# Performance work log

Measured on AMD Instinct MI355X. Metric: run time of the kernel, lower is better.

## Reference

```python
import jax, jax.numpy as jnp
import numpy as np

N_USER = 150_000
M_ITEM = 30_000
N_NODES = N_USER + M_ITEM
D = 64                      # embedding_dim
N_LAYERS = 3                # gcn_layer_number
E = 600_000                 # user-item interactions (symmetric nnz = 2E)
B = 1024
NUM_RATE, NUM_GENRE, NUM_DIR, NUM_ACT = 6, 25, 2186, 8030
NUM_GENDER, NUM_AGE, NUM_OCC, NUM_ZIP = 2, 7, 21, 3402
H1, H2 = 64, 64             # first/second fc hidden dims
FC1_IN = D * 10


def setup_inputs() -> dict:
    key = jax.random.key(0)
    ks = jax.random.split(key, 24)
    # aux features: 0/1 values are valid indices for every categorical field
    aux_info = jax.random.randint(ks[0], (B, 10246), 0, 2, dtype=jnp.int32)
    user_ids = jax.random.randint(ks[1], (B,), 0, N_USER, dtype=jnp.int32)
    item_ids = jax.random.randint(ks[2], (B,), 0, M_ITEM, dtype=jnp.int32)
    # bipartite graph: random interactions, symmetric normalized adjacency
    u = jax.random.randint(ks[3], (E,), 0, N_USER, dtype=jnp.int32)
    i = jax.random.randint(ks[4], (E,), 0, M_ITEM, dtype=jnp.int32) + N_USER
    graph_row = jnp.concatenate([u, i])
    graph_col = jnpph = jnp.concatenate([i, u]) if False else jnp.concatenate([i, u])
    deg = jax.ops.segment_sum(jnp.ones((2 * E,), jnp.float32), graph_row, num_segments=N_NODES)
    dinv = jnp.where(deg > 0, jax.lax.rsqrt(jnp.maximum(deg, 1.0)), 0.0)
    graph_val = dinv[graph_row] * dinv[graph_col]
    s = 0.1
    nrm = lambda k, shp: (jax.random.normal(k, shp, jnp.float32) * s)
    return {
        "aux_info": aux_info, "user_ids": user_ids, "item_ids": item_ids,
        "graph_row": graph_row, "graph_col": graph_col, "graph_val": graph_val,
        "rate_tab": nrm(ks[5], (NUM_RATE, D)),
        "genre_W": nrm(ks[6], (NUM_GENRE, D)),
        "director_W": nrm(ks[7], (NUM_DIR, D)),
        "actor_W": nrm(ks[8], (NUM_ACT, D)),
        "gender_tab": nrm(ks[9], (NUM_GENDER, D)),
        "age_tab": nrm(ks[10], (NUM_AGE, D)),
        "occ_tab": nrm(ks[11], (NUM_OCC, D)),
        "area_tab": nrm(ks[12], (NUM_ZIP, D)),
        "user_rel": nrm(ks[13], (N_USER, D)),
        "item_rel": nrm(ks[14], (M_ITEM, D)),
        "fc1_W": nrm(ks[15], (FC1_IN, H1)), "fc1_b": jnp.zeros((H1,), jnp.float32),
        "fc2_W": nrm(ks[16], (H1, H2)), "fc2_b": jnp.zeros((H2,), jnp.float32),
        "out_W": nrm(ks[17], (H2, 1)), "out_b": jnp.zeros((1,), jnp.float32),
    }


def _lightgcn(user_rel, item_rel, row, col, val):
    # LightGCN: repeated SpMM D^-1/2 A D^-1/2 @ emb, mean over layer outputs
    emb = jnp.concatenate([user_rel, item_rel], axis=0)      # [N, D]
    acc = emb
    for _ in range(N_LAYERS):
        emb = jax.ops.segment_sum(val[:, None] * emb[col], row, num_segments=N_NODES)
        acc = acc + emb
    light = acc / (N_LAYERS + 1)
    return light[:N_USER], light[N_USER:]


def _multi_hot(idx_int, W):
    x = idx_int.astype(jnp.float32)
    return (x @ W) / jnp.sum(x, axis=1, keepdims=True)


def reference(aux_info, user_ids, item_ids, graph_row, graph_col, graph_val,
              rate_tab, genre_W, director_W, actor_W,
              gender_tab, age_tab, occ_tab, area_tab,
              user_rel, item_rel,
              fc1_W, fc1_b, fc2_W, fc2_b, out_W, out_b):
    rate_idx = aux_info[:, 0]
    genre_idx = aux_info[:, 1:26]
    director_idx = aux_info[:, 26:2212]
    actor_idx = aux_info[:, 2212:10242]
    gender_idx = aux_info[:, 10242]
    age_idx = aux_info[:, 10243]
    occ_idx = aux_info[:, 10244]
    area_idx = aux_info[:, 10245]

    item_emb = jnp.concatenate([
        rate_tab[rate_idx],
        _multi_hot(genre_idx, genre_W),
        _multi_hot(director_idx, director_W),
        _multi_hot(actor_idx, actor_W),
    ], axis=1)                                               # [B, 4D]
    user_emb = jnp.concatenate([
        gender_tab[gender_idx], age_tab[age_idx],
        occ_tab[occ_idx], area_tab[area_idx],
    ], axis=1)                                               # [B, 4D]

    all_users, all_items = _lightgcn(user_rel, item_rel, graph_row, graph_col, graph_val)
    X = jnp.concatenate([item_emb, user_emb,
                         all_users[user_ids], all_items[item_ids]], axis=1)  # [B, 10D]
    X = jax.nn.relu(X @ fc1_W + fc1_b)
    X = jax.nn.relu(X @ fc2_W + fc2_b)
    return X @ out_W + out_b                                 # [B, 1]
```

## Files before the change

kernel.cpp:

```cpp
#include <hip/hip_runtime.h>
#include <hip/hip_bf16.h>
#include <hip/hip_fp16.h>

#define N_USER 150000
#define M_ITEM 30000
#define N_NODES 180000
#define E2 1200000
#define BATCH 1024
#define AUX_W 10246
#define KP_G 32
#define KP_D 2208
#define KP_A 8064
#define NBKT 265

typedef __attribute__((ext_vector_type(8))) short short8;
typedef __attribute__((ext_vector_type(4))) float f32x4;

__device__ __forceinline__ int bucket_of(int r) {
    return r < N_USER ? (r >> 10) : 147 + ((r - N_USER) >> 8);
}

__device__ __forceinline__ int detect_f32(const void* probe) {
    float v = __bfloat162float(((const __hip_bfloat16*)probe)[threadIdx.x & 63]);
    unsigned long long m = __ballot(!(fabsf(v) < 1000.0f));
    return __popcll(m) > 8;
}

struct CvtSeg { const void* src; float* dst; int n; int blk0; };
struct CvtBatch { CvtSeg seg[16]; };

__global__ void __launch_bounds__(256) k_cvt_batch(CvtBatch cb, const void* probe) {
    int isf32 = detect_f32(probe);
    int blk = blockIdx.x;
    int si = 0;
    #pragma unroll
    for (int i = 0; i < 16; ++i) if (blk >= cb.seg[i].blk0) si = i;
    const CvtSeg sg = cb.seg[si];
    int i = (blk - sg.blk0) * 256 + threadIdx.x;
    if (i >= sg.n) return;
    if (isf32) sg.dst[i] = ((const float*)sg.src)[i];
    else       sg.dst[i] = __bfloat162float(((const __hip_bfloat16*)sg.src)[i]);
}

__global__ void __launch_bounds__(256) k_cvt_emb(const void* rawU, const void* rawI,
                                                 const float* __restrict__ dinv,
                                                 __half* __restrict__ emb,
                                                 float* __restrict__ tacc,
                                                 const int* __restrict__ uids,
                                                 const int* __restrict__ iids, int cvtN) {
    int isf32 = detect_f32(rawU);
    if ((int)blockIdx.x >= cvtN) {
        int lane = threadIdx.x & 63;
        int t = (blockIdx.x - cvtN) * 4 + (threadIdx.x >> 6);
        const void* src; size_t ri;
        if (t < BATCH) { src = rawU; ri = (size_t)uids[t]; }
        else           { src = rawI; ri = (size_t)iids[t - BATCH]; }
        float v;
        if (isf32) v = ((const float*)src)[ri * 64 + lane];
        else       v = __bfloat162float(((const __hip_bfloat16*)src)[ri * 64 + lane]);
        tacc[(size_t)t * 64 + lane] = v;
        return;
    }
    int q = blockIdx.x * 256 + threadIdx.x;
    if (q >= N_NODES * 16) return;
    int r = q >> 4;
    const void* src; size_t qq;
    if (r < N_USER) { src = rawU; qq = (size_t)q; }
    else            { src = rawI; qq = (size_t)q - (size_t)N_USER * 16; }
    float d = dinv[r];
    float4 v;
    if (isf32) {
        v = ((const float4*)src)[qq];
    } else {
        ushort4 u = ((const ushort4*)src)[qq];
        v.x = __bfloat162float(*(__hip_bfloat16*)&u.x);
        v.y = __bfloat162float(*(__hip_bfloat16*)&u.y);
        v.z = __bfloat162float(*(__hip_bfloat16*)&u.z);
        v.w = __bfloat162float(*(__hip_bfloat16*)&u.w);
    }
    __half h0 = __float2half(v.x * d), h1 = __float2half(v.y * d);
    __half h2 = __float2half(v.z * d), h3 = __float2half(v.w * d);
    ushort4 o = { *(unsigned short*)&h0, *(unsigned short*)&h1,
                  *(unsigned short*)&h2, *(unsigned short*)&h3 };
    ((ushort4*)emb)[(size_t)q] = o;
}

__global__ void __launch_bounds__(256) k_wt(const void* Wg, const void* Wd, const void* Wa,
                                            unsigned short* WtG, unsigned short* WtD, unsigned short* WtA,
                                            const void* probe) {
    int isf32 = detect_f32(probe);
    int t = blockIdx.x * 256 + threadIdx.x;
    if (t >= (KP_G + KP_D + KP_A) * 64) return;
    int kp = t >> 6, n = t & 63;
    int k, K; const void* src; unsigned short* dst;
    if (kp < KP_G)              { k = kp;                K = 25;   src = Wg; dst = WtG; }
    else if (kp < KP_G + KP_D)  { k = kp - KP_G;         K = 2186; src = Wd; dst = WtD; }
    else                        { k = kp - KP_G - KP_D;  K = 8030; src = Wa; dst = WtA; }
    unsigned short v = 0;
    if (k < K) {
        if (isf32) {
            __hip_bfloat16 h = __float2bfloat16(((const float*)src)[(size_t)k * 64 + n]);
            v = *(unsigned short*)&h;
        } else {
            v = ((const unsigned short*)src)[(size_t)k * 64 + n];
        }
    }
    dst[(((size_t)(k >> 5) * 64 + n) * 4 + ((k >> 3) & 3)) * 8 + (k & 7)] = v;
}

__global__ void __launch_bounds__(256) k_zero(int* p, int n) {
    int i = blockIdx.x * 256 + threadIdx.x;
    if (i < n) p[i] = 0;
}

__global__ void __launch_bounds__(256) k_bcnt(const int* __restrict__ grow, int* __restrict__ bucket_tot) {
    __shared__ int h[NBKT];
    int tid = threadIdx.x;
    for (int i = tid; i < NBKT; i += 256) h[i] = 0;
    __syncthreads();
    int idx0 = blockIdx.x * 4096;
    #pragma unroll
    for (int k = 0; k < 16; ++k) {
        int i = idx0 + k * 256 + tid;
        if (i < E2) atomicAdd(&h[bucket_of(grow[i])], 1);
    }
    __syncthreads();
    for (int i = tid; i < NBKT; i += 256) if (h[i]) atomicAdd(&bucket_tot[i], h[i]);
}

__global__ void __launch_bounds__(512) k_bscan(const int* __restrict__ bucket_tot,
                                               int* __restrict__ bucket_base,
                                               int* __restrict__ bucketcur,
                                               int* __restrict__ offs) {
    __shared__ int s[512];
    int tid = threadIdx.x;
    s[tid] = (tid < NBKT) ? bucket_tot[tid] : 0;
    __syncthreads();
    for (int off = 1; off < 512; off <<= 1) {
        int v = (tid >= off) ? s[tid - off] : 0;
        __syncthreads();
        s[tid] += v;
        __syncthreads();
    }
    int excl = tid ? s[tid - 1] : 0;
    bucket_base[tid] = excl;
    if (tid < NBKT) bucketcur[tid] = excl;
    if (tid == 0) offs[N_NODES] = E2;
}

__global__ void __launch_bounds__(256) k_p1(const int* __restrict__ grow, const int* __restrict__ gcol,
                                            int* __restrict__ bucketcur, int2* __restrict__ binned) {
    __shared__ int h1[NBKT], base1[NBKT];
    int tid = threadIdx.x;
    for (int i = tid; i < NBKT; i += 256) h1[i] = 0;
    __syncthreads();
    int idx0 = blockIdx.x * 4096;
    int r[16], c[16];
    #pragma unroll
    for (int k = 0; k < 16; ++k) {
        int i = idx0 + k * 256 + tid;
        if (i < E2) {
            r[k] = grow[i]; c[k] = gcol[i];
            atomicAdd(&h1[bucket_of(r[k])], 1);
        } else r[k] = -1;
    }
    __syncthreads();
    for (int i = tid; i < NBKT; i += 256) {
        base1[i] = h1[i] ? atomicAdd(&bucketcur[i], h1[i]) : 0;
        h1[i] = 0;
    }
    __syncthreads();
    #pragma unroll
    for (int k = 0; k < 16; ++k) {
        if (r[k] >= 0) {
            int b = bucket_of(r[k]);
            int p = base1[b] + atomicAdd(&h1[b], 1);
            binned[p] = make_int2(r[k], c[k]);
        }
    }
}

__global__ void __launch_bounds__(256) k_p2(const int2* __restrict__ binned, const int* __restrict__ bb,
                                            int* __restrict__ cols, int* __restrict__ offs,
                                            float* __restrict__ dinv, float* __restrict__ dsq,
                                            float* __restrict__ gsc) {
    __shared__ int h[1024];
    __shared__ int ws2[256];
    int b = blockIdx.x, tid = threadIdx.x;
    int r0, r1;
    if (b < 147) { r0 = b << 10; r1 = min((b + 1) << 10, N_USER); }
    else         { r0 = N_USER + ((b - 147) << 8); r1 = min(N_USER + ((b - 146) << 8), N_NODES); }
    int s0 = bb[b], e0 = bb[b + 1];
    for (int i = tid; i < 1024; i += 256) h[i] = 0;
    __syncthreads();
    for (int j = s0 + tid; j < e0; j += 256) atomicAdd(&h[binned[j].x - r0], 1);
    __syncthreads();
    int t0 = tid * 4;
    int a0 = h[t0], a1 = h[t0 + 1], a2 = h[t0 + 2], a3 = h[t0 + 3];
    ws2[tid] = a0 + a1 + a2 + a3;
    __syncthreads();
    for (int off = 1; off < 256; off <<= 1) {
        int v = (tid >= off) ? ws2[tid - off] : 0;
        __syncthreads();
        ws2[tid] += v;
        __syncthreads();
    }
    int excl = tid ? ws2[tid - 1] : 0;
    int ex[4] = { excl, excl + a0, excl + a0 + a1, excl + a0 + a1 + a2 };
    int ac[4] = { a0, a1, a2, a3 };
    #pragma unroll
    for (int i = 0; i < 4; ++i) {
        int row = r0 + t0 + i;
        if (row < r1) {
            offs[row] = s0 + ex[i];
            float deg = (float)ac[i];
            bool nz = deg > 0.f;
            dinv[row] = nz ? rsqrtf(deg) : 0.f;
            dsq[row]  = nz ? 1.f / deg  : 0.f;
            gsc[row]  = nz ? sqrtf(deg) : 0.f;
        }
        h[t0 + i] = ex[i];
    }
    __syncthreads();
    for (int j = s0 + tid; j < e0; j += 256) {
        int2 e = binned[j];
        int p = s0 + atomicAdd(&h[e.x - r0], 1);
        cols[p] = e.y << 7;
    }
}

__global__ void __launch_bounds__(256) k_mark(const int* __restrict__ offs, const int* __restrict__ cols,
                                              const int* __restrict__ uids, const int* __restrict__ iids,
                                              int* __restrict__ mark, int* __restrict__ mark2) {
    int lane = threadIdx.x & 63;
    int t = blockIdx.x * 4 + (threadIdx.x >> 6);
    if (t >= 2048) return;
    int r = (t < BATCH) ? uids[t] : (N_USER + iids[t - BATCH]);
    if (lane == 0) { mark[r] = 1; mark2[r] = 1; }
    int s = offs[r], e = offs[r + 1];
    for (int j = s + lane; j < e; j += 64) mark[(unsigned)cols[j] >> 7] = 1;
}

__global__ void __launch_bounds__(256) k_mark2(const int* __restrict__ offs, const int* __restrict__ cols,
                                               const int* __restrict__ mark, int* __restrict__ mark2) {
    int lane = threadIdx.x & 63;
    int wid = blockIdx.x * 4 + (threadIdx.x >> 6);
    if (wid >= N_NODES) return;
    if (mark[wid] == 0) return;
    int s = offs[wid], e = offs[wid + 1];
    for (int j = s + lane; j < e; j += 64) mark2[(unsigned)cols[j] >> 7] = 1;
}

__global__ void __launch_bounds__(256, 8) k_spmv(const __half* __restrict__ src, __half* __restrict__ dst,
                                                 const int* __restrict__ offs, const int* __restrict__ cols,
                                                 const float* __restrict__ dsq, const int* __restrict__ mark,
                                                 int spmvN, float* __restrict__ tacc,
                                                 const int* __restrict__ uids, const int* __restrict__ iids,
                                                 const float* __restrict__ gsc) {
    int tid = threadIdx.x, lane = tid & 63;
    int blk = blockIdx.x;
    if (blk >= spmvN) {
        int t = (blk - spmvN) * 4 + (tid >> 6);
        int r = (t < BATCH) ? uids[t] : (N_USER + iids[t - BATCH]);
        tacc[(size_t)t * 64 + lane] += __half2float(src[(size_t)r * 64 + lane]) * gsc[r];
        return;
    }
    int wid = blk * 4 + (tid >> 6);
    if (wid >= N_NODES) return;
    if (mark && mark[wid] == 0) return;
    int s = offs[wid], e = offs[wid + 1];
    int p = lane & 31, ep = lane >> 5;
    const char* sb = (const char*)src + (p << 2);
    float ax = 0.f, ay = 0.f;
    int j0 = s;
    for (; j0 + 16 <= e; j0 += 16) {
        int c[8];
        #pragma unroll
        for (int u = 0; u < 8; ++u) c[u] = cols[j0 + 2 * u + ep];
        float2 v[8];
        #pragma unroll
        for (int u = 0; u < 8; ++u) v[u] = __half22float2(*(const __half2*)(sb + (size_t)(unsigned)c[u]));
        #pragma unroll
        for (int u = 0; u < 8; ++u) { ax += v[u].x; ay += v[u].y; }
    }
    if (j0 < e) {
        int c[8]; float w[8];
        #pragma unroll
        for (int u = 0; u < 8; ++u) {
            int j = j0 + 2 * u + ep;
            c[u] = cols[min(j, e - 1)];
            w[u] = (j < e) ? 1.f : 0.f;
        }
        float2 v[8];
        #pragma unroll
        for (int u = 0; u < 8; ++u) v[u] = __half22float2(*(const __half2*)(sb + (size_t)(unsigned)c[u]));
        #pragma unroll
        for (int u = 0; u < 8; ++u) { ax = fmaf(w[u], v[u].x, ax); ay = fmaf(w[u], v[u].y, ay); }
    }
    ax += __shfl_xor(ax, 32);
    ay += __shfl_xor(ay, 32);
    if (ep == 0) {
        float d = dsq[wid];
        *(__half2*)((char*)dst + ((size_t)wid << 7) + (p << 2)) = __floats2half2_rn(ax * d, ay * d);
    }
}

__global__ void __launch_bounds__(256) k_spmv3(const __half* __restrict__ src, float* __restrict__ tacc,
                                               const int* __restrict__ offs, const int* __restrict__ cols,
                                               const float* __restrict__ dinv, const float* __restrict__ gsc,
                                               const int* __restrict__ uids, const int* __restrict__ iids) {
    int tid = threadIdx.x, lane = tid & 63;
    int t = blockIdx.x * 4 + (tid >> 6);
    if (t >= 2048) return;
    int r = (t < BATCH) ? uids[t] : (N_USER + iids[t - BATCH]);
    int s = offs[r], e = offs[r + 1];
    int p = lane & 31, ep = lane >> 5;
    const char* sb = (const char*)src + (p << 2);
    float ax = 0.f, ay = 0.f;
    int j0 = s;
    for (; j0 + 16 <= e; j0 += 16) {
        int c[8];
        #pragma unroll
        for (int u = 0; u < 8; ++u) c[u] = cols[j0 + 2 * u + ep];
        float2 v[8];
        #pragma unroll
        for (int u = 0; u < 8; ++u) v[u] = __half22float2(*(const __half2*)(sb + (size_t)(unsigned)c[u]));
        #pragma unroll
        for (int u = 0; u < 8; ++u) { ax += v[u].x; ay += v[u].y; }
    }
    if (j0 < e) {
        int c[8]; float w[8];
        #pragma unroll
        for (int u = 0; u < 8; ++u) {
            int j = j0 + 2 * u + ep;
            c[u] = cols[min(j, e - 1)];
            w[u] = (j < e) ? 1.f : 0.f;
        }
        float2 v[8];
        #pragma unroll
        for (int u = 0; u < 8; ++u) v[u] = __half22float2(*(const __half2*)(sb + (size_t)(unsigned)c[u]));
        #pragma unroll
        for (int u = 0; u < 8; ++u) { ax = fmaf(w[u], v[u].x, ax); ay = fmaf(w[u], v[u].y, ay); }
    }
    ax += __shfl_xor(ax, 32);
    ay += __shfl_xor(ay, 32);
    if (ep == 0) {
        float2 self = __half22float2(*(const __half2*)((const char*)src + ((size_t)r << 7) + (p << 2)));
        float di = dinv[r], g = gsc[r];
        float* tp = tacc + (size_t)t * 64 + (p << 1);
        tp[0] += di * ax + g * self.x;
        tp[1] += di * ay + g * self.y;
    }
}

__global__ void __launch_bounds__(256) k_mhgemm(const int* __restrict__ aux,
                                                const unsigned short* __restrict__ WtG,
                                                const unsigned short* __restrict__ WtD,
                                                const unsigned short* __restrict__ WtA,
                                                float* __restrict__ Xmh, float* __restrict__ cntf) {
    int blk = blockIdx.x;
    int seg, rb, k0, klen, Kseg, auxoff;
    const unsigned short* Wt;
    if (blk < 16)      { seg = 0; rb = blk;                      k0 = 0;              klen = 25;                    Kseg = 25;   auxoff = 1;    Wt = WtG; }
    else if (blk < 96) { int t = blk - 16; seg = 1; rb = t & 15; k0 = (t >> 4) * 512; klen = min(512, 2186 - k0);   Kseg = 2186; auxoff = 26;   Wt = WtD; }
    else               { int t = blk - 96; seg = 2; rb = t & 15; k0 = (t >> 4) * 512; klen = min(512, 8030 - k0);   Kseg = 8030; auxoff = 2212; Wt = WtA; }
    int lane = threadIdx.x & 63, wave = threadIdx.x >> 6;
    int m = lane & 15, quad = lane >> 4;
    int row = rb * 64 + wave * 16 + m;
    const int* arow = aux + (size_t)row * AUX_W + auxoff;

    f32x4 acc0 = {0.f,0.f,0.f,0.f}, acc1 = acc0, acc2 = acc0, acc3 = acc0;
    float asum = 0.f;
    int nchunk = (klen + 31) >> 5;
    for (int kci = 0; kci < nchunk; ++kci) {
        int kb = k0 + kci * 32 + quad * 8;
        short8 af;
        if (kb + 8 <= Kseg) {
            #pragma unroll
            for (int j = 0; j < 8; ++j) {
                int x = arow[kb + j];
                af[j] = x ? (short)0x3F80 : (short)0;
                asum += (float)x;
            }
        } else {
            #pragma unroll
            for (int j = 0; j < 8; ++j) {
                int x = (kb + j < Kseg) ? arow[kb + j] : 0;
                af[j] = x ? (short)0x3F80 : (short)0;
                asum += (float)x;
            }
        }
        size_t kcg = (size_t)(k0 >> 5) + kci;
        const unsigned short* bp = Wt + ((kcg * 64 + m) * 4 + quad) * 8;
        short8 b0 = *(const short8*)(bp);
        short8 b1 = *(const short8*)(bp + 512);
        short8 b2 = *(const short8*)(bp + 1024);
        short8 b3 = *(const short8*)(bp + 1536);
        acc0 = __builtin_amdgcn_mfma_f32_16x16x32_bf16(af, b0, acc0, 0, 0, 0);
        acc1 = __builtin_amdgcn_mfma_f32_16x16x32_bf16(af, b1, acc1, 0, 0, 0);
        acc2 = __builtin_amdgcn_mfma_f32_16x16x32_bf16(af, b2, acc2, 0, 0, 0);
        acc3 = __builtin_amdgcn_mfma_f32_16x16x32_bf16(af, b3, acc3, 0, 0, 0);
    }
    asum += __shfl_xor(asum, 16);
    asum += __shfl_xor(asum, 32);
    if (quad == 0) atomicAdd(&cntf[seg * BATCH + row], asum);
    float* xbase = Xmh + ((size_t)seg * BATCH + rb * 64 + wave * 16 + quad * 4) * 64;
    #pragma unroll
    for (int reg = 0; reg < 4; ++reg) {
        float* xr = xbase + (size_t)reg * 64;
        atomicAdd(&xr[ 0 + m], acc0[reg]);
        atomicAdd(&xr[16 + m], acc1[reg]);
        atomicAdd(&xr[32 + m], acc2[reg]);
        atomicAdd(&xr[48 + m], acc3[reg]);
    }
}

__global__ void __launch_bounds__(256) k_mlp(const int* __restrict__ aux,
                                             const float* __restrict__ ratef, const float* __restrict__ genderf,
                                             const float* __restrict__ agef, const float* __restrict__ occf,
                                             const float* __restrict__ areaf, const float* __restrict__ tacc,
                                             const float* __restrict__ Xmh, const float* __restrict__ cntf,
                                             const float* __restrict__ W1, const float* __restrict__ b1,
                                             const float* __restrict__ W2, const float* __restrict__ b2,
                                             const float* __restrict__ Wo, const float* __restrict__ bo,
                                             void* __restrict__ out, const void* probe) {
    __shared__ float sx[4][640];
    __shared__ float sh[4][64];
    int isf32 = detect_f32(probe);
    int lane = threadIdx.x & 63, w = threadIdx.x >> 6;
    int b = blockIdx.x * 4 + w;
    const int* arow = aux + (size_t)b * AUX_W;
    float* xr = sx[w];
    xr[0   + lane] = ratef[arow[0] * 64 + lane];
    xr[64  + lane] = Xmh[((size_t)0 * BATCH + b) * 64 + lane] / cntf[0 * BATCH + b];
    xr[128 + lane] = Xmh[((size_t)1 * BATCH + b) * 64 + lane] / cntf[1 * BATCH + b];
    xr[192 + lane] = Xmh[((size_t)2 * BATCH + b) * 64 + lane] / cntf[2 * BATCH + b];
    xr[256 + lane] = genderf[arow[10242] * 64 + lane];
    xr[320 + lane] = agef[arow[10243] * 64 + lane];
    xr[384 + lane] = occf[arow[10244] * 64 + lane];
    xr[448 + lane] = areaf[arow[10245] * 64 + lane];
    xr[512 + lane] = tacc[(size_t)b * 64 + lane] * 0.25f;
    xr[576 + lane] = tacc[(size_t)(BATCH + b) * 64 + lane] * 0.25f;
    float acc = b1[lane];
    #pragma unroll 8
    for (int k = 0; k < 640; ++k) acc += xr[k] * W1[(size_t)k * 64 + lane];
    float h1 = fmaxf(acc, 0.f);
    sh[w][lane] = h1;
    float acc2 = b2[lane];
    #pragma unroll 8
    for (int j = 0; j < 64; ++j) acc2 += sh[w][j] * W2[(size_t)j * 64 + lane];
    float h2 = fmaxf(acc2, 0.f);
    float p = h2 * Wo[lane];
    #pragma unroll
    for (int off = 32; off; off >>= 1) p += __shfl_down(p, off);
    if (lane == 0) {
        float r = p + bo[0];
        if (isf32) ((float*)out)[b] = r;
        else       ((__hip_bfloat16*)out)[b] = __float2bfloat16(r);
    }
}

extern "C" void kernel_launch(void* const* d_in, const int* in_sizes, int n_in,
                              void* d_out, int out_size, void* d_ws, size_t ws_size,
                              hipStream_t stream) {
    const int* aux  = (const int*)d_in[0];
    const int* uids = (const int*)d_in[1];
    const int* iids = (const int*)d_in[2];
    const int* grow = (const int*)d_in[3];
    const int* gcol = (const int*)d_in[4];

    char* p = (char*)d_ws;
    auto alloc = [&](size_t bytes) -> char* {
        char* r = p;
        p += (bytes + 255) / 256 * 256;
        return r;
    };
    int*   mark        = (int*)alloc((size_t)180224 * 4);
    int*   mark2       = (int*)alloc((size_t)180224 * 4);
    int*   bucket_tot  = (int*)alloc(512 * 4);
    float* Xmh         = (float*)alloc((size_t)3 * BATCH * 64 * 4);
    float* cntf        = (float*)alloc((size_t)3 * BATCH * 4);
    const int ZERO_N   = 180224 + 180224 + 512 + 3 * BATCH * 64 + 3 * BATCH;
    int*   bucket_base = (int*)alloc(512 * 4);
    int*   bucketcur   = (int*)alloc(512 * 4);
    int*   offs        = (int*)alloc((size_t)180224 * 4);
    float* dinv        = (float*)alloc((size_t)180224 * 4);
    float* dsq         = (float*)alloc((size_t)180224 * 4);
    float* gsc         = (float*)alloc((size_t)180224 * 4);
    int2*  binned      = (int2*)alloc((size_t)E2 * 8);
    int*   cols        = (int*)alloc((size_t)E2 * 4);
    __half* embA       = (__half*)alloc((size_t)N_NODES * 64 * 2);
    __half* embB       = (__half*)alloc((size_t)N_NODES * 64 * 2);
    float* tacc        = (float*)alloc((size_t)2048 * 64 * 4);
    unsigned short* WtG = (unsigned short*)alloc((size_t)KP_G * 64 * 2);
    unsigned short* WtD = (unsigned short*)alloc((size_t)KP_D * 64 * 2);
    unsigned short* WtA = (unsigned short*)alloc((size_t)KP_A * 64 * 2);
    float* ratef   = (float*)alloc(384 * 4);
    float* genderf = (float*)alloc(128 * 4);
    float* agef    = (float*)alloc(448 * 4);
    float* occf    = (float*)alloc(1344 * 4);
    float* areaf   = (float*)alloc((size_t)217728 * 4);
    float* fc1W    = (float*)alloc((size_t)40960 * 4);
    float* fc1b    = (float*)alloc(64 * 4);
    float* fc2W    = (float*)alloc(4096 * 4);
    float* fc2b    = (float*)alloc(64 * 4);
    float* outW    = (float*)alloc(64 * 4);
    float* outb    = (float*)alloc(4);

    const void* probe = d_in[14];

    CvtBatch cb;
    int blk = 0, si = 0;
    auto addseg = [&](const void* s, float* d, int n) {
        cb.seg[si].src = s; cb.seg[si].dst = d; cb.seg[si].n = n; cb.seg[si].blk0 = blk;
        blk += (n + 255) / 256; ++si;
    };
    addseg(d_in[6],  ratef,   384);
    addseg(d_in[10], genderf, 128);
    addseg(d_in[11], agef,    448);
    addseg(d_in[12], occf,    1344);
    addseg(d_in[13], areaf,   217728);
    addseg(d_in[16], fc1W,   40960);
    addseg(d_in[17], fc1b,   64);
    addseg(d_in[18], fc2W,   4096);
    addseg(d_in[19], fc2b,   64);
    addseg(d_in[20], outW,   64);
    addseg(d_in[21], outb,   1);
    for (int i = si; i < 16; ++i) { cb.seg[i].src = nullptr; cb.seg[i].dst = nullptr; cb.seg[i].n = 0; cb.seg[i].blk0 = 0x7fffffff; }
    hipLaunchKernelGGL(k_cvt_batch, dim3(blk), dim3(256), 0, stream, cb, probe);

    hipLaunchKernelGGL(k_wt, dim3(((KP_G + KP_D + KP_A) * 64 + 255) / 256), dim3(256), 0, stream,
                       d_in[7], d_in[8], d_in[9], WtG, WtD, WtA, probe);

    hipLaunchKernelGGL(k_zero, dim3((ZERO_N + 255) / 256), dim3(256), 0, stream, mark, ZERO_N);

    hipLaunchKernelGGL(k_bcnt, dim3((E2 + 4095) / 4096), dim3(256), 0, stream, grow, bucket_tot);
    hipLaunchKernelGGL(k_bscan, dim3(1), dim3(512), 0, stream, bucket_tot, bucket_base, bucketcur, offs);
    hipLaunchKernelGGL(k_p1, dim3((E2 + 4095) / 4096), dim3(256), 0, stream, grow, gcol, bucketcur, binned);
    hipLaunchKernelGGL(k_p2, dim3(NBKT), dim3(256), 0, stream, binned, bucket_base, cols, offs, dinv, dsq, gsc);

    const int cvtN = (N_NODES * 16 + 255) / 256;
    hipLaunchKernelGGL(k_cvt_emb, dim3(cvtN + 512), dim3(256), 0, stream,
                       d_in[14], d_in[15], dinv, embA, tacc, uids, iids, cvtN);
    hipLaunchKernelGGL(k_mark, dim3(2048 / 4), dim3(256), 0, stream, offs, cols, uids, iids, mark, mark2);
    hipLaunchKernelGGL(k_mark2, dim3((N_NODES + 3) / 4), dim3(256), 0, stream, offs, cols, mark, mark2);

    const int spmvN = (N_NODES + 3) / 4;
    hipLaunchKernelGGL(k_spmv, dim3(spmvN), dim3(256), 0, stream,
                       embA, embB, offs, cols, dsq, mark2, spmvN, (float*)nullptr, uids, iids, gsc);
    hipLaunchKernelGGL(k_spmv, dim3(spmvN + 512), dim3(256), 0, stream,
                       embB, embA, offs, cols, dsq, mark, spmvN, tacc, uids, iids, gsc);
    hipLaunchKernelGGL(k_spmv3, dim3(2048 / 4), dim3(256), 0, stream,
                       embA, tacc, offs, cols, dinv, gsc, uids, iids);

    hipLaunchKernelGGL(k_mhgemm, dim3(352), dim3(256), 0, stream, aux, WtG, WtD, WtA, Xmh, cntf);
    hipLaunchKernelGGL(k_mlp, dim3(BATCH / 4), dim3(256), 0, stream,
                       aux, ratef, genderf, agef, occf, areaf, tacc, Xmh, cntf,
                       fc1W, fc1b, fc2W, fc2b, outW, outb, d_out, probe);
}
```

Measured before the change: 356.1 us.

## Fuse prep kernels and replace mark arrays with per-row start/end offsets

Merges the scalar-table conversion, weight transpose and bucket count into one prep kernel, and swaps the zero kernel for a memset. Row offsets are now stored as int2 start/end pairs, so the frontier masks for the pruned SpMV layers can be written as copied offsets in a second array, with empty ranges for skipped rows. The embedding conversion, frontier marking and the multi-hot GEMM now run in one fused launch. The aim is fewer launches and serialization points, at the cost of larger offset arrays and more complex block dispatch.

```diff
diff --git a/kernel.cpp b/kernel.cpp
--- a/kernel.cpp
+++ b/kernel.cpp
@@ -12,6 +12,8 @@
 #define KP_D 2208
 #define KP_A 8064
 #define NBKT 265
+#define WT_BLKS 2576
+#define BCNT_BLKS 293
 
 typedef __attribute__((ext_vector_type(8))) short short8;
 typedef __attribute__((ext_vector_type(4))) float f32x4;
@@ -29,96 +31,49 @@
 struct CvtSeg { const void* src; float* dst; int n; int blk0; };
 struct CvtBatch { CvtSeg seg[16]; };
 
-__global__ void __launch_bounds__(256) k_cvt_batch(CvtBatch cb, const void* probe) {
-    int isf32 = detect_f32(probe);
-    int blk = blockIdx.x;
-    int si = 0;
-    #pragma unroll
-    for (int i = 0; i < 16; ++i) if (blk >= cb.seg[i].blk0) si = i;
-    const CvtSeg sg = cb.seg[si];
-    int i = (blk - sg.blk0) * 256 + threadIdx.x;
-    if (i >= sg.n) return;
-    if (isf32) sg.dst[i] = ((const float*)sg.src)[i];
-    else       sg.dst[i] = __bfloat162float(((const __hip_bfloat16*)sg.src)[i]);
-}
-
-__global__ void __launch_bounds__(256) k_cvt_emb(const void* rawU, const void* rawI,
-                                                 const float* __restrict__ dinv,
-                                                 __half* __restrict__ emb,
-                                                 float* __restrict__ tacc,
-                                                 const int* __restrict__ uids,
-                                                 const int* __restrict__ iids, int cvtN) {
-    int isf32 = detect_f32(rawU);
-    if ((int)blockIdx.x >= cvtN) {
-        int lane = threadIdx.x & 63;
-        int t = (blockIdx.x - cvtN) * 4 + (threadIdx.x >> 6);
-        const void* src; size_t ri;
-        if (t < BATCH) { src = rawU; ri = (size_t)uids[t]; }
-        else           { src = rawI; ri = (size_t)iids[t - BATCH]; }
-        float v;
-        if (isf32) v = ((const float*)src)[ri * 64 + lane];
-        else       v = __bfloat162float(((const __hip_bfloat16*)src)[ri * 64 + lane]);
-        tacc[(size_t)t * 64 + lane] = v;
+__global__ void __launch_bounds__(256) k_prep(CvtBatch cb, int cvtBlks,
+                                              const void* Wg, const void* Wd, const void* Wa,
+                                              unsigned short* WtG, unsigned short* WtD, unsigned short* WtA,
+                                              const int* __restrict__ grow, int* __restrict__ bucket_tot,
+                                              const void* probe) {
+    int blk = blockIdx.x, tid = threadIdx.x;
+    if (blk < cvtBlks) {
+        int isf32 = detect_f32(probe);
+        int si = 0;
+        #pragma unroll
+        for (int i = 0; i < 16; ++i) if (blk >= cb.seg[i].blk0) si = i;
+        const CvtSeg sg = cb.seg[si];
+        int i = (blk - sg.blk0) * 256 + tid;
+        if (i >= sg.n) return;
+        if (isf32) sg.dst[i] = ((const float*)sg.src)[i];
+        else       sg.dst[i] = __bfloat162float(((const __hip_bfloat16*)sg.src)[i]);
         return;
     }
-    int q = blockIdx.x * 256 + threadIdx.x;
-    if (q >= N_NODES * 16) return;
-    int r = q >> 4;
-    const void* src; size_t qq;
-    if (r < N_USER) { src = rawU; qq = (size_t)q; }
-    else            { src = rawI; qq = (size_t)q - (size_t)N_USER * 16; }
-    float d = dinv[r];
-    float4 v;
-    if (isf32) {
-        v = ((const float4*)src)[qq];
-    } else {
-        ushort4 u = ((const ushort4*)src)[qq];
-        v.x = __bfloat162float(*(__hip_bfloat16*)&u.x);
-        v.y = __bfloat162float(*(__hip_bfloat16*)&u.y);
-        v.z = __bfloat162float(*(__hip_bfloat16*)&u.z);
-        v.w = __bfloat162float(*(__hip_bfloat16*)&u.w);
-    }
-    __half h0 = __float2half(v.x * d), h1 = __float2half(v.y * d);
-    __half h2 = __float2half(v.z * d), h3 = __float2half(v.w * d);
-    ushort4 o = { *(unsigned short*)&h0, *(unsigned short*)&h1,
-                  *(unsigned short*)&h2, *(unsigned short*)&h3 };
-    ((ushort4*)emb)[(size_t)q] = o;
-}
-
-__global__ void __launch_bounds__(256) k_wt(const void* Wg, const void* Wd, const void* Wa,
-                                            unsigned short* WtG, unsigned short* WtD, unsigned short* WtA,
-                                            const void* probe) {
-    int isf32 = detect_f32(probe);
-    int t = blockIdx.x * 256 + threadIdx.x;
-    if (t >= (KP_G + KP_D + KP_A) * 64) return;
-    int kp = t >> 6, n = t & 63;
-    int k, K; const void* src; unsigned short* dst;
-    if (kp < KP_G)              { k = kp;                K = 25;   src = Wg; dst = WtG; }
-    else if (kp < KP_G + KP_D)  { k = kp - KP_G;         K = 2186; src = Wd; dst = WtD; }
-    else                        { k = kp - KP_G - KP_D;  K = 8030; src = Wa; dst = WtA; }
-    unsigned short v = 0;
-    if (k < K) {
-        if (isf32) {
-            __hip_bfloat16 h = __float2bfloat16(((const float*)src)[(size_t)k * 64 + n]);
-            v = *(unsigned short*)&h;
-        } else {
-            v = ((const unsigned short*)src)[(size_t)k * 64 + n];
-        }
-    }
-    dst[(((size_t)(k >> 5) * 64 + n) * 4 + ((k >> 3) & 3)) * 8 + (k & 7)] = v;
-}
-
-__global__ void __launch_bounds__(256) k_zero(int* p, int n) {
-    int i = blockIdx.x * 256 + threadIdx.x;
-    if (i < n) p[i] = 0;
-}
-
-__global__ void __launch_bounds__(256) k_bcnt(const int* __restrict__ grow, int* __restrict__ bucket_tot) {
+    if (blk < cvtBlks + WT_BLKS) {
+        int isf32 = detect_f32(probe);
+        int t = (blk - cvtBlks) * 256 + tid;
+        if (t >= (KP_G + KP_D + KP_A) * 64) return;
+        int kp = t >> 6, n = t & 63;
+        int k, K; const void* src; unsigned short* dst;
+        if (kp < KP_G)              { k = kp;               K = 25;   src = Wg; dst = WtG; }
+        else if (kp < KP_G + KP_D)  { k = kp - KP_G;        K = 2186; src = Wd; dst = WtD; }
+        else                        { k = kp - KP_G - KP_D; K = 8030; src = Wa; dst = WtA; }
+        unsigned short v = 0;
+        if (k < K) {
+            if (isf32) {
+                __hip_bfloat16 h = __float2bfloat16(((const float*)src)[(size_t)k * 64 + n]);
+                v = *(unsigned short*)&h;
+            } else {
+                v = ((const unsigned short*)src)[(size_t)k * 64 + n];
+            }
+        }
+        dst[(((size_t)(k >> 5) * 64 + n) * 4 + ((k >> 3) & 3)) * 8 + (k & 7)] = v;
+        return;
+    }
     __shared__ int h[NBKT];
-    int tid = threadIdx.x;
     for (int i = tid; i < NBKT; i += 256) h[i] = 0;
     __syncthreads();
-    int idx0 = blockIdx.x * 4096;
+    int idx0 = (blk - cvtBlks - WT_BLKS) * 4096;
     #pragma unroll
     for (int k = 0; k < 16; ++k) {
         int i = idx0 + k * 256 + tid;
@@ -130,8 +85,7 @@
 
 __global__ void __launch_bounds__(512) k_bscan(const int* __restrict__ bucket_tot,
                                                int* __restrict__ bucket_base,
-                                               int* __restrict__ bucketcur,
-                                               int* __restrict__ offs) {
+                                               int* __restrict__ bucketcur) {
     __shared__ int s[512];
     int tid = threadIdx.x;
     s[tid] = (tid < NBKT) ? bucket_tot[tid] : 0;
@@ -145,7 +99,6 @@
     int excl = tid ? s[tid - 1] : 0;
     bucket_base[tid] = excl;
     if (tid < NBKT) bucketcur[tid] = excl;
-    if (tid == 0) offs[N_NODES] = E2;
 }
 
 __global__ void __launch_bounds__(256) k_p1(const int* __restrict__ grow, const int* __restrict__ gcol,
@@ -181,7 +134,7 @@
 }
 
 __global__ void __launch_bounds__(256) k_p2(const int2* __restrict__ binned, const int* __restrict__ bb,
-                                            int* __restrict__ cols, int* __restrict__ offs,
+                                            int* __restrict__ cols, int2* __restrict__ moffs,
                                             float* __restrict__ dinv, float* __restrict__ dsq,
                                             float* __restrict__ gsc) {
     __shared__ int h[1024];
@@ -212,7 +165,7 @@
     for (int i = 0; i < 4; ++i) {
         int row = r0 + t0 + i;
         if (row < r1) {
-            offs[row] = s0 + ex[i];
+            moffs[row] = make_int2(s0 + ex[i], s0 + ex[i] + ac[i]);
             float deg = (float)ac[i];
             bool nz = deg > 0.f;
             dinv[row] = nz ? rsqrtf(deg) : 0.f;
@@ -229,141 +182,16 @@
     }
 }
 
-__global__ void __launch_bounds__(256) k_mark(const int* __restrict__ offs, const int* __restrict__ cols,
-                                              const int* __restrict__ uids, const int* __restrict__ iids,
-                                              int* __restrict__ mark, int* __restrict__ mark2) {
-    int lane = threadIdx.x & 63;
-    int t = blockIdx.x * 4 + (threadIdx.x >> 6);
-    if (t >= 2048) return;
-    int r = (t < BATCH) ? uids[t] : (N_USER + iids[t - BATCH]);
-    if (lane == 0) { mark[r] = 1; mark2[r] = 1; }
-    int s = offs[r], e = offs[r + 1];
-    for (int j = s + lane; j < e; j += 64) mark[(unsigned)cols[j] >> 7] = 1;
-}
-
-__global__ void __launch_bounds__(256) k_mark2(const int* __restrict__ offs, const int* __restrict__ cols,
-                                               const int* __restrict__ mark, int* __restrict__ mark2) {
-    int lane = threadIdx.x & 63;
-    int wid = blockIdx.x * 4 + (threadIdx.x >> 6);
-    if (wid >= N_NODES) return;
-    if (mark[wid] == 0) return;
-    int s = offs[wid], e = offs[wid + 1];
-    for (int j = s + lane; j < e; j += 64) mark2[(unsigned)cols[j] >> 7] = 1;
-}
-
-__global__ void __launch_bounds__(256, 8) k_spmv(const __half* __restrict__ src, __half* __restrict__ dst,
-                                                 const int* __restrict__ offs, const int* __restrict__ cols,
-                                                 const float* __restrict__ dsq, const int* __restrict__ mark,
-                                                 int spmvN, float* __restrict__ tacc,
-                                                 const int* __restrict__ uids, const int* __restrict__ iids,
-                                                 const float* __restrict__ gsc) {
-    int tid = threadIdx.x, lane = tid & 63;
-    int blk = blockIdx.x;
-    if (blk >= spmvN) {
-        int t = (blk - spmvN) * 4 + (tid >> 6);
-        int r = (t < BATCH) ? uids[t] : (N_USER + iids[t - BATCH]);
-        tacc[(size_t)t * 64 + lane] += __half2float(src[(size_t)r * 64 + lane]) * gsc[r];
-        return;
-    }
-    int wid = blk * 4 + (tid >> 6);
-    if (wid >= N_NODES) return;
-    if (mark && mark[wid] == 0) return;
-    int s = offs[wid], e = offs[wid + 1];
-    int p = lane & 31, ep = lane >> 5;
-    const char* sb = (const char*)src + (p << 2);
-    float ax = 0.f, ay = 0.f;
-    int j0 = s;
-    for (; j0 + 16 <= e; j0 += 16) {
-        int c[8];
-        #pragma unroll
-        for (int u = 0; u < 8; ++u) c[u] = cols[j0 + 2 * u + ep];
-        float2 v[8];
-        #pragma unroll
-        for (int u = 0; u < 8; ++u) v[u] = __half22float2(*(const __half2*)(sb + (size_t)(unsigned)c[u]));
-        #pragma unroll
-        for (int u = 0; u < 8; ++u) { ax += v[u].x; ay += v[u].y; }
-    }
-    if (j0 < e) {
-        int c[8]; float w[8];
-        #pragma unroll
-        for (int u = 0; u < 8; ++u) {
-            int j = j0 + 2 * u + ep;
-            c[u] = cols[min(j, e - 1)];
-            w[u] = (j < e) ? 1.f : 0.f;
-        }
-        float2 v[8];
-        #pragma unroll
-        for (int u = 0; u < 8; ++u) v[u] = __half22float2(*(const __half2*)(sb + (size_t)(unsigned)c[u]));
-        #pragma unroll
-        for (int u = 0; u < 8; ++u) { ax = fmaf(w[u], v[u].x, ax); ay = fmaf(w[u], v[u].y, ay); }
-    }
-    ax += __shfl_xor(ax, 32);
-    ay += __shfl_xor(ay, 32);
-    if (ep == 0) {
-        float d = dsq[wid];
-        *(__half2*)((char*)dst + ((size_t)wid << 7) + (p << 2)) = __floats2half2_rn(ax * d, ay * d);
-    }
-}
-
-__global__ void __launch_bounds__(256) k_spmv3(const __half* __restrict__ src, float* __restrict__ tacc,
-                                               const int* __restrict__ offs, const int* __restrict__ cols,
-                                               const float* __restrict__ dinv, const float* __restrict__ gsc,
-                                               const int* __restrict__ uids, const int* __restrict__ iids) {
-    int tid = threadIdx.x, lane = tid & 63;
-    int t = blockIdx.x * 4 + (tid >> 6);
-    if (t >= 2048) return;
-    int r = (t < BATCH) ? uids[t] : (N_USER + iids[t - BATCH]);
-    int s = offs[r], e = offs[r + 1];
-    int p = lane & 31, ep = lane >> 5;
-    const char* sb = (const char*)src + (p << 2);
-    float ax = 0.f, ay = 0.f;
-    int j0 = s;
-    for (; j0 + 16 <= e; j0 += 16) {
-        int c[8];
-        #pragma unroll
-        for (int u = 0; u < 8; ++u) c[u] = cols[j0 + 2 * u + ep];
-        float2 v[8];
-        #pragma unroll
-        for (int u = 0; u < 8; ++u) v[u] = __half22float2(*(const __half2*)(sb + (size_t)(unsigned)c[u]));
-        #pragma unroll
-        for (int u = 0; u < 8; ++u) { ax += v[u].x; ay += v[u].y; }
-    }
-    if (j0 < e) {
-        int c[8]; float w[8];
-        #pragma unroll
-        for (int u = 0; u < 8; ++u) {
-            int j = j0 + 2 * u + ep;
-            c[u] = cols[min(j, e - 1)];
-            w[u] = (j < e) ? 1.f : 0.f;
-        }
-        float2 v[8];
-        #pragma unroll
-        for (int u = 0; u < 8; ++u) v[u] = __half22float2(*(const __half2*)(sb + (size_t)(unsigned)c[u]));
-        #pragma unroll
-        for (int u = 0; u < 8; ++u) { ax = fmaf(w[u], v[u].x, ax); ay = fmaf(w[u], v[u].y, ay); }
-    }
-    ax += __shfl_xor(ax, 32);
-    ay += __shfl_xor(ay, 32);
-    if (ep == 0) {
-        float2 self = __half22float2(*(const __half2*)((const char*)src + ((size_t)r << 7) + (p << 2)));
-        float di = dinv[r], g = gsc[r];
-        float* tp = tacc + (size_t)t * 64 + (p << 1);
-        tp[0] += di * ax + g * self.x;
-        tp[1] += di * ay + g * self.y;
-    }
-}
-
-__global__ void __launch_bounds__(256) k_mhgemm(const int* __restrict__ aux,
-                                                const unsigned short* __restrict__ WtG,
-                                                const unsigned short* __restrict__ WtD,
-                                                const unsigned short* __restrict__ WtA,
-                                                float* __restrict__ Xmh, float* __restrict__ cntf) {
-    int blk = blockIdx.x;
+__device__ void mhgemm_body(int blk, const int* __restrict__ aux,
+                            const unsigned short* __restrict__ WtG,
+                            const unsigned short* __restrict__ WtD,
+                            const unsigned short* __restrict__ WtA,
+                            float* __restrict__ Xmh, float* __restrict__ cntf) {
     int seg, rb, k0, klen, Kseg, auxoff;
     const unsigned short* Wt;
-    if (blk < 16)      { seg = 0; rb = blk;                      k0 = 0;              klen = 25;                    Kseg = 25;   auxoff = 1;    Wt = WtG; }
-    else if (blk < 96) { int t = blk - 16; seg = 1; rb = t & 15; k0 = (t >> 4) * 512; klen = min(512, 2186 - k0);   Kseg = 2186; auxoff = 26;   Wt = WtD; }
-    else               { int t = blk - 96; seg = 2; rb = t & 15; k0 = (t >> 4) * 512; klen = min(512, 8030 - k0);   Kseg = 8030; auxoff = 2212; Wt = WtA; }
+    if (blk < 16)      { seg = 0; rb = blk;                      k0 = 0;              klen = 25;                  Kseg = 25;   auxoff = 1;    Wt = WtG; }
+    else if (blk < 96) { int t = blk - 16; seg = 1; rb = t & 15; k0 = (t >> 4) * 512; klen = min(512, 2186 - k0); Kseg = 2186; auxoff = 26;   Wt = WtD; }
+    else               { int t = blk - 96; seg = 2; rb = t & 15; k0 = (t >> 4) * 512; klen = min(512, 8030 - k0); Kseg = 8030; auxoff = 2212; Wt = WtA; }
     int lane = threadIdx.x & 63, wave = threadIdx.x >> 6;
     int m = lane & 15, quad = lane >> 4;
     int row = rb * 64 + wave * 16 + m;
@@ -412,6 +240,178 @@
         atomicAdd(&xr[16 + m], acc1[reg]);
         atomicAdd(&xr[32 + m], acc2[reg]);
         atomicAdd(&xr[48 + m], acc3[reg]);
+    }
+}
+
+__global__ void __launch_bounds__(256) k_cvt_fused(const void* rawU, const void* rawI,
+                                                   const float* __restrict__ dinv,
+                                                   __half* __restrict__ emb,
+                                                   float* __restrict__ tacc,
+                                                   const int* __restrict__ uids,
+                                                   const int* __restrict__ iids, int cvtN,
+                                                   const int2* __restrict__ moffs,
+                                                   const int* __restrict__ cols,
+                                                   int2* __restrict__ moffs2,
+                                                   const int* __restrict__ aux,
+                                                   const unsigned short* __restrict__ WtG,
+                                                   const unsigned short* __restrict__ WtD,
+                                                   const unsigned short* __restrict__ WtA,
+                                                   float* __restrict__ Xmh, float* __restrict__ cntf) {
+    int blk = blockIdx.x;
+    if (blk >= cvtN + 1024) {
+        mhgemm_body(blk - cvtN - 1024, aux, WtG, WtD, WtA, Xmh, cntf);
+        return;
+    }
+    if (blk >= cvtN + 512) {
+        int lane = threadIdx.x & 63;
+        int t = (blk - cvtN - 512) * 4 + (threadIdx.x >> 6);
+        int r = (t < BATCH) ? uids[t] : (N_USER + iids[t - BATCH]);
+        int2 se = moffs[r];
+        if (lane == 0) moffs2[r] = se;
+        for (int j = se.x + lane; j < se.y; j += 64) {
+            int c = (unsigned)cols[j] >> 7;
+            moffs2[c] = moffs[c];
+        }
+        return;
+    }
+    int isf32 = detect_f32(rawU);
+    if (blk >= cvtN) {
+        int lane = threadIdx.x & 63;
+        int t = (blk - cvtN) * 4 + (threadIdx.x >> 6);
+        const void* src; size_t ri;
+        if (t < BATCH) { src = rawU; ri = (size_t)uids[t]; }
+        else           { src = rawI; ri = (size_t)iids[t - BATCH]; }
+        float v;
+        if (isf32) v = ((const float*)src)[ri * 64 + lane];
+        else       v = __bfloat162float(((const __hip_bfloat16*)src)[ri * 64 + lane]);
+        tacc[(size_t)t * 64 + lane] = v;
+        return;
+    }
+    int q = blk * 256 + threadIdx.x;
+    if (q >= N_NODES * 16) return;
+    int r = q >> 4;
+    const void* src; size_t qq;
+    if (r < N_USER) { src = rawU; qq = (size_t)q; }
+    else            { src = rawI; qq = (size_t)q - (size_t)N_USER * 16; }
+    float d = dinv[r];
+    float4 v;
+    if (isf32) {
+        v = ((const float4*)src)[qq];
+    } else {
+        ushort4 u = ((const ushort4*)src)[qq];
+        v.x = __bfloat162float(*(__hip_bfloat16*)&u.x);
+        v.y = __bfloat162float(*(__hip_bfloat16*)&u.y);
+        v.z = __bfloat162float(*(__hip_bfloat16*)&u.z);
+        v.w = __bfloat162float(*(__hip_bfloat16*)&u.w);
+    }
+    __half h0 = __float2half(v.x * d), h1 = __float2half(v.y * d);
+    __half h2 = __float2half(v.z * d), h3 = __float2half(v.w * d);
+    ushort4 o = { *(unsigned short*)&h0, *(unsigned short*)&h1,
+                  *(unsigned short*)&h2, *(unsigned short*)&h3 };
+    ((ushort4*)emb)[(size_t)q] = o;
+}
+
+__global__ void __launch_bounds__(256, 8) k_spmv(const __half* __restrict__ src, __half* __restrict__ dst,
+                                                 const int2* __restrict__ moffs_in, const int* __restrict__ cols,
+                                                 const float* __restrict__ dsq,
+                                                 int spmvN, float* __restrict__ tacc,
+                                                 const int* __restrict__ uids, const int* __restrict__ iids,
+                                                 const float* __restrict__ gsc) {
+    int tid = threadIdx.x, lane = tid & 63;
+    int blk = blockIdx.x;
+    if (blk >= spmvN) {
+        int t = (blk - spmvN) * 4 + (tid >> 6);
+        int r = (t < BATCH) ? uids[t] : (N_USER + iids[t - BATCH]);
+        tacc[(size_t)t * 64 + lane] += __half2float(src[(size_t)r * 64 + lane]) * gsc[r];
+        return;
+    }
+    int wid = blk * 4 + (tid >> 6);
+    if (wid >= N_NODES) return;
+    int2 se = moffs_in[wid];
+    int s = se.x, e = se.y;
+    if (e <= s) return;
+    int p = lane & 31, ep = lane >> 5;
+    const char* sb = (const char*)src + (p << 2);
+    float ax = 0.f, ay = 0.f;
+    int j0 = s;
+    for (; j0 + 16 <= e; j0 += 16) {
+        int c[8];
+        #pragma unroll
+        for (int u = 0; u < 8; ++u) c[u] = cols[j0 + 2 * u + ep];
+        float2 v[8];
+        #pragma unroll
+        for (int u = 0; u < 8; ++u) v[u] = __half22float2(*(const __half2*)(sb + (size_t)(unsigned)c[u]));
+        #pragma unroll
+        for (int u = 0; u < 8; ++u) { ax += v[u].x; ay += v[u].y; }
+    }
+    if (j0 < e) {
+        int c[8]; float w[8];
+        #pragma unroll
+        for (int u = 0; u < 8; ++u) {
+            int j = j0 + 2 * u + ep;
+            c[u] = cols[min(j, e - 1)];
+            w[u] = (j < e) ? 1.f : 0.f;
+        }
+        float2 v[8];
+        #pragma unroll
+        for (int u = 0; u < 8; ++u) v[u] = __half22float2(*(const __half2*)(sb + (size_t)(unsigned)c[u]));
+        #pragma unroll
+        for (int u = 0; u < 8; ++u) { ax = fmaf(w[u], v[u].x, ax); ay = fmaf(w[u], v[u].y, ay); }
+    }
+    ax += __shfl_xor(ax, 32);
+    ay += __shfl_xor(ay, 32);
+    if (ep == 0) {
+        float d = dsq[wid];
+        *(__half2*)((char*)dst + ((size_t)wid << 7) + (p << 2)) = __floats2half2_rn(ax * d, ay * d);
+    }
+}
+
+__global__ void __launch_bounds__(256) k_spmv3(const __half* __restrict__ src, float* __restrict__ tacc,
+                                               const int2* __restrict__ moffs, const int* __restrict__ cols,
+                                               const float* __restrict__ dinv, const float* __restrict__ gsc,
+                                               const int* __restrict__ uids, const int* __restrict__ iids) {
+    int tid = threadIdx.x, lane = tid & 63;
+    int t = blockIdx.x * 4 + (tid >> 6);
+    if (t >= 2048) return;
+    int r = (t < BATCH) ? uids[t] : (N_USER + iids[t - BATCH]);
+    int2 se = moffs[r];
+    int s = se.x, e = se.y;
+    int p = lane & 31, ep = lane >> 5;
+    const char* sb = (const char*)src + (p << 2);
+    float ax = 0.f, ay = 0.f;
+    int j0 = s;
+    for (; j0 + 16 <= e; j0 += 16) {
+        int c[8];
+        #pragma unroll
+        for (int u = 0; u < 8; ++u) c[u] = cols[j0 + 2 * u + ep];
+        float2 v[8];
+        #pragma unroll
+        for (int u = 0; u < 8; ++u) v[u] = __half22float2(*(const __half2*)(sb + (size_t)(unsigned)c[u]));
+        #pragma unroll
+        for (int u = 0; u < 8; ++u) { ax += v[u].x; ay += v[u].y; }
+    }
+    if (j0 < e) {
+        int c[8]; float w[8];
+        #pragma unroll
+        for (int u = 0; u < 8; ++u) {
+            int j = j0 + 2 * u + ep;
+            c[u] = cols[min(j, e - 1)];
+            w[u] = (j < e) ? 1.f : 0.f;
+        }
+        float2 v[8];
+        #pragma unroll
+        for (int u = 0; u < 8; ++u) v[u] = __half22float2(*(const __half2*)(sb + (size_t)(unsigned)c[u]));
+        #pragma unroll
+        for (int u = 0; u < 8; ++u) { ax = fmaf(w[u], v[u].x, ax); ay = fmaf(w[u], v[u].y, ay); }
+    }
+    ax += __shfl_xor(ax, 32);
+    ay += __shfl_xor(ay, 32);
+    if (ep == 0) {
+        float2 self = __half22float2(*(const __half2*)((const char*)src + ((size_t)r << 7) + (p << 2)));
+        float di = dinv[r], g = gsc[r];
+        float* tp = tacc + (size_t)t * 64 + (p << 1);
+        tp[0] += di * ax + g * self.x;
+        tp[1] += di * ay + g * self.y;
     }
 }
 
@@ -475,15 +475,14 @@
         p += (bytes + 255) / 256 * 256;
         return r;
     };
-    int*   mark        = (int*)alloc((size_t)180224 * 4);
-    int*   mark2       = (int*)alloc((size_t)180224 * 4);
     int*   bucket_tot  = (int*)alloc(512 * 4);
     float* Xmh         = (float*)alloc((size_t)3 * BATCH * 64 * 4);
     float* cntf        = (float*)alloc((size_t)3 * BATCH * 4);
-    const int ZERO_N   = 180224 + 180224 + 512 + 3 * BATCH * 64 + 3 * BATCH;
+    int2*  moffs2      = (int2*)alloc((size_t)180224 * 8);
+    char*  zero_end    = p;
     int*   bucket_base = (int*)alloc(512 * 4);
     int*   bucketcur   = (int*)alloc(512 * 4);
-    int*   offs        = (int*)alloc((size_t)180224 * 4);
+    int2*  moffs       = (int2*)alloc((size_t)180224 * 8);
     float* dinv        = (float*)alloc((size_t)180224 * 4);
     float* dsq         = (float*)alloc((size_t)180224 * 4);
     float* gsc         = (float*)alloc((size_t)180224 * 4);
@@ -509,6 +508,8 @@
 
     const void* probe = d_in[14];
 
+    hipMemsetAsync(bucket_tot, 0, (size_t)(zero_end - (char*)bucket_tot), stream);
+
     CvtBatch cb;
     int blk = 0, si = 0;
     auto addseg = [&](const void* s, float* d, int n) {
@@ -527,33 +528,27 @@
     addseg(d_in[20], outW,   64);
     addseg(d_in[21], outb,   1);
     for (int i = si; i < 16; ++i) { cb.seg[i].src = nullptr; cb.seg[i].dst = nullptr; cb.seg[i].n = 0; cb.seg[i].blk0 = 0x7fffffff; }
-    hipLaunchKernelGGL(k_cvt_batch, dim3(blk), dim3(256), 0, stream, cb, probe);
-
-    hipLaunchKernelGGL(k_wt, dim3(((KP_G + KP_D + KP_A) * 64 + 255) / 256), dim3(256), 0, stream,
-                       d_in[7], d_in[8], d_in[9], WtG, WtD, WtA, probe);
-
-    hipLaunchKernelGGL(k_zero, dim3((ZERO_N + 255) / 256), dim3(256), 0, stream, mark, ZERO_N);
-
-    hipLaunchKernelGGL(k_bcnt, dim3((E2 + 4095) / 4096), dim3(256), 0, stream, grow, bucket_tot);
-    hipLaunchKernelGGL(k_bscan, dim3(1), dim3(512), 0, stream, bucket_tot, bucket_base, bucketcur, offs);
+    const int cvtBlks = blk;
+    hipLaunchKernelGGL(k_prep, dim3(cvtBlks + WT_BLKS + BCNT_BLKS), dim3(256), 0, stream,
+                       cb, cvtBlks, d_in[7], d_in[8], d_in[9], WtG, WtD, WtA, grow, bucket_tot, probe);
+
+    hipLaunchKernelGGL(k_bscan, dim3(1), dim3(512), 0, stream, bucket_tot, bucket_base, bucketcur);
     hipLaunchKernelGGL(k_p1, dim3((E2 + 4095) / 4096), dim3(256), 0, stream, grow, gcol, bucketcur, binned);
-    hipLaunchKernelGGL(k_p2, dim3(NBKT), dim3(256), 0, stream, binned, bucket_base, cols, offs, dinv, dsq, gsc);
+    hipLaunchKernelGGL(k_p2, dim3(NBKT), dim3(256), 0, stream, binned, bucket_base, cols, moffs, dinv, dsq, gsc);
 
     const int cvtN = (N_NODES * 16 + 255) / 256;
-    hipLaunchKernelGGL(k_cvt_emb, dim3(cvtN + 512), dim3(256), 0, stream,
-                       d_in[14], d_in[15], dinv, embA, tacc, uids, iids, cvtN);
-    hipLaunchKernelGGL(k_mark, dim3(2048 / 4), dim3(256), 0, stream, offs, cols, uids, iids, mark, mark2);
-    hipLaunchKernelGGL(k_mark2, dim3((N_NODES + 3) / 4), dim3(256), 0, stream, offs, cols, mark, mark2);
+    hipLaunchKernelGGL(k_cvt_fused, dim3(cvtN + 1024 + 352), dim3(256), 0, stream,
+                       d_in[14], d_in[15], dinv, embA, tacc, uids, iids, cvtN,
+                       moffs, cols, moffs2, aux, WtG, WtD, WtA, Xmh, cntf);
 
     const int spmvN = (N_NODES + 3) / 4;
     hipLaunchKernelGGL(k_spmv, dim3(spmvN), dim3(256), 0, stream,
-                       embA, embB, offs, cols, dsq, mark2, spmvN, (float*)nullptr, uids, iids, gsc);
+                       embA, embB, moffs, cols, dsq, spmvN, (float*)nullptr, uids, iids, gsc);
     hipLaunchKernelGGL(k_spmv, dim3(spmvN + 512), dim3(256), 0, stream,
-                       embB, embA, offs, cols, dsq, mark, spmvN, tacc, uids, iids, gsc);
+                       embB, embA, moffs2, cols, dsq, spmvN, tacc, uids, iids, gsc);
     hipLaunchKernelGGL(k_spmv3, dim3(2048 / 4), dim3(256), 0, stream,
-                       embA, tacc, offs, cols, dinv, gsc, uids, iids);
-
-    hipLaunchKernelGGL(k_mhgemm, dim3(352), dim3(256), 0, stream, aux, WtG, WtD, WtA, Xmh, cntf);
+                       embA, tacc, moffs, cols, dinv, gsc, uids, iids);
+
     hipLaunchKernelGGL(k_mlp, dim3(BATCH / 4), dim3(256), 0, stream,
                        aux, ratef, genderf, agef, occf, areaf, tacc, Xmh, cntf,
                        fc1W, fc1b, fc2W, fc2b, outW, outb, d_out, probe);
```

Measured after the change: 353.4 us. Within noise of the previous version (-0.7%).
